# Kernel tuning notes

Measured on AMD Instinct MI355X. Metric: run time of the kernel, lower is better.

## Reference

```python
import jax, jax.numpy as jnp
import numpy as np

B, T, F, H = 256, 1024, 64, 128
DT = 1.0
EPS = 1e-5


def _layer_norm(h, g, b):
    mu = jnp.mean(h, axis=-1, keepdims=True)
    var = jnp.var(h, axis=-1, keepdims=True)
    return (h - mu) * jax.lax.rsqrt(var + EPS) * g + b


def setup_inputs() -> dict:
    key = jax.random.key(0)
    ks = jax.random.split(key, 8)
    def xavier(k, shape):
        fan_in, fan_out = shape[1], shape[0]
        lim = np.sqrt(6.0 / (fan_in + fan_out))
        return jax.random.uniform(k, shape, jnp.float32, -lim, lim)
    return {
        "x": jax.random.normal(ks[0], (B, T, F), jnp.float32),
        # layer 0 (input_dim=F)
        "Wh0": xavier(ks[1], (H, H)), "bh0": jnp.zeros((H,), jnp.float32),
        "Wx0": xavier(ks[2], (H, F)), "bx0": jnp.zeros((H,), jnp.float32),
        "Wt0": xavier(ks[3], (H, F)), "bt0": jnp.zeros((H,), jnp.float32),
        "tau0": jnp.ones((H,), jnp.float32),
        "g0": jnp.ones((H,), jnp.float32), "be0": jnp.zeros((H,), jnp.float32),
        # layer 1 (input_dim=H)
        "Wh1": xavier(ks[4], (H, H)), "bh1": jnp.zeros((H,), jnp.float32),
        "Wx1": xavier(ks[5], (H, H)), "bx1": jnp.zeros((H,), jnp.float32),
        "Wt1": xavier(ks[6], (H, H)), "bt1": jnp.zeros((H,), jnp.float32),
        "tau1": jnp.ones((H,), jnp.float32),
        "g1": jnp.ones((H,), jnp.float32), "be1": jnp.zeros((H,), jnp.float32),
    }


def _cell(x_t, h, Wh, bh, Wx, bx, Wt, bt, tau_base):
    f = jnp.tanh(h @ Wh.T + bh + x_t @ Wx.T + bx)        # (B,H)
    tau = tau_base + jax.nn.softplus(x_t @ Wt.T + bt)     # (B,H)
    return h + (DT / tau) * (-h + f)


def reference(x, Wh0, bh0, Wx0, bx0, Wt0, bt0, tau0, g0, be0,
              Wh1, bh1, Wx1, bx1, Wt1, bt1, tau1, g1, be1):
    xT = jnp.transpose(x, (1, 0, 2))  # (T,B,F)

    def step(carry, x_t):
        h0, h1 = carry
        h0 = _layer_norm(_cell(x_t, h0, Wh0, bh0, Wx0, bx0, Wt0, bt0, tau0), g0, be0)
        h1 = _layer_norm(_cell(h0, h1, Wh1, bh1, Wx1, bx1, Wt1, bt1, tau1), g1, be1)
        return (h0, h1), None

    h_init = (jnp.zeros((x.shape[0], H), x.dtype), jnp.zeros((x.shape[0], H), x.dtype))
    (h0, h1), _ = jax.lax.scan(step, h_init, xT)
    return h1  # hidden_dim == latent_dim, no proj
```

## Files before the change

kernel.cpp:

```cpp
#include <hip/hip_runtime.h>
#include <stdint.h>


#define B_ 256
#define T_ 1024
#define F_ 64
#define H_ 128
#define EPS_ 1e-5f
#define NT_ 512

typedef _Float16 h2 __attribute__((ext_vector_type(2)));
typedef _Float16 h8 __attribute__((ext_vector_type(8)));
typedef float f32x4 __attribute__((ext_vector_type(4)));
typedef __fp16  f16v2 __attribute__((ext_vector_type(2)));

__device__ __forceinline__ h2 pkf16(float a, float b) {
  union { f16v2 f; h2 h; } c;
  c.f = __builtin_amdgcn_cvt_pkrtz(a, b);
  return c.h;
}
__device__ __forceinline__ uint32_t as_u32(h2 h) { union { h2 h; uint32_t u; } c; c.h = h; return c.u; }

__device__ __forceinline__ void wg_barrier() {
  asm volatile("s_waitcnt lgkmcnt(0)\n\ts_barrier" ::: "memory");
}

#if __has_builtin(__builtin_amdgcn_rsqf)
__device__ __forceinline__ float rsq_fast(float x) { return __builtin_amdgcn_rsqf(x); }
#else
__device__ __forceinline__ float rsq_fast(float x) { return rsqrtf(x); }
#endif

#if __has_builtin(__builtin_amdgcn_update_dpp)
template <int CTRL>
__device__ __forceinline__ float dpp_add(float v) {
  union { float f; int i; } a, b;
  a.f = v;
  b.i = __builtin_amdgcn_update_dpp(0, a.i, CTRL, 0xf, 0xf, true);
  return v + b.f;
}
__device__ __forceinline__ float red16(float v) {
  v = dpp_add<0x128>(v);
  v = dpp_add<0x124>(v);
  v = dpp_add<0x122>(v);
  v = dpp_add<0x121>(v);
  return v;
}
#else
__device__ __forceinline__ float red16(float v) {
  v += __shfl_xor(v, 1); v += __shfl_xor(v, 2);
  v += __shfl_xor(v, 4); v += __shfl_xor(v, 8);
  return v;
}
#endif

__device__ __forceinline__ h8 packfrag(const float* p) {
  float4 a = *(const float4*)p;
  float4 b = *(const float4*)(p + 4);
  union { h2 h[4]; h8 v; } c;
  c.h[0] = pkf16(a.x, a.y); c.h[1] = pkf16(a.z, a.w);
  c.h[2] = pkf16(b.x, b.y); c.h[3] = pkf16(b.z, b.w);
  return c.v;
}
__device__ __forceinline__ h8 packfrag_g(const float* w, const float* gv, const float* bv,
                                         float& dg, float& dbe) {
  float4 a = *(const float4*)w;
  float4 b = *(const float4*)(w + 4);
  float4 ga = *(const float4*)gv;
  float4 gb = *(const float4*)(gv + 4);
  float4 ba = *(const float4*)bv;
  float4 bb = *(const float4*)(bv + 4);
  float w0 = a.x*ga.x, w1 = a.y*ga.y, w2 = a.z*ga.z, w3 = a.w*ga.w;
  float w4 = b.x*gb.x, w5 = b.y*gb.y, w6 = b.z*gb.z, w7 = b.w*gb.w;
  dg  += (w0 + w1) + (w2 + w3) + (w4 + w5) + (w6 + w7);
  dbe += a.x*ba.x + a.y*ba.y + a.z*ba.z + a.w*ba.w
       + b.x*bb.x + b.y*bb.y + b.z*bb.z + b.w*bb.w;
  union { h2 h[4]; h8 v; } c;
  c.h[0] = pkf16(w0, w1); c.h[1] = pkf16(w2, w3);
  c.h[2] = pkf16(w4, w5); c.h[3] = pkf16(w6, w7);
  return c.v;
}
__device__ __forceinline__ h8 ldfrag(const uint32_t* p) {
  union { uint4 u; h8 v; } c;
  c.u = *(const uint4*)p;
  return c.v;
}

__device__ __forceinline__ float tanh_fast(float a) {
  float aa = fabsf(a);
  float e  = __expf(2.f * aa);
  float th = 1.f - 2.f * __builtin_amdgcn_rcpf(e + 1.f);
  return copysignf(th, a);
}
__device__ __forceinline__ float softplus_fast(float x) {
  return (x > 20.f) ? x : __logf(1.f + __expf(x));
}

#define MFMA16(A_, B_, C_) __builtin_amdgcn_mfma_f32_16x16x32_f16(A_, B_, C_, 0, 0, 0)

__global__ void __attribute__((amdgpu_flat_work_group_size(NT_, NT_)))
                __attribute__((amdgpu_waves_per_eu(2, 2)))
ltc_scan(
    const float* __restrict__ x,
    const float* __restrict__ Wh0, const float* __restrict__ bh0,
    const float* __restrict__ Wx0, const float* __restrict__ bx0,
    const float* __restrict__ Wt0, const float* __restrict__ bt0,
    const float* __restrict__ tau0, const float* __restrict__ g0,
    const float* __restrict__ be0,
    const float* __restrict__ Wh1, const float* __restrict__ bh1,
    const float* __restrict__ Wx1, const float* __restrict__ bx1,
    const float* __restrict__ Wt1, const float* __restrict__ bt1,
    const float* __restrict__ tau1, const float* __restrict__ g1,
    const float* __restrict__ be1,
    float* __restrict__ out)
{
  __shared__ __align__(16) uint32_t h0p[2][64];
  __shared__ __align__(16) uint32_t h1p[2][64];
  __shared__ __align__(16) uint32_t hn0p[4][64];
  __shared__ __align__(16) uint32_t x4[4][32];
  __shared__ __align__(16) float2   p0s[4][4];
  __shared__ __align__(16) float2   p1s[4][4];

  const int tid = threadIdx.x;
  const int wid = tid >> 6;
  const int l   = tid & 63;
  const int g4  = (l >> 4) << 2;
  const int g8  = (l >> 4) << 3;
  const int b   = blockIdx.x;
  const float* xg = x + (size_t)b * (T_ * F_);
  const bool selT1 = (l & 16) != 0;

  if (tid < 128) { ((uint32_t*)h0p)[tid] = 0u; ((uint32_t*)h1p)[tid] = 0u; }
  if (tid < 32)  { ((float*)p0s)[tid] = 0.f; ((float*)p1s)[tid] = 0.f; }
  if (tid < 32) {
    float2 a = *(const float2*)(xg + 2 * tid);
    float2 c = *(const float2*)(xg + F_ + 2 * tid);
    x4[0][tid] = as_u32(pkf16(a.x, a.y));
    x4[1][tid] = as_u32(pkf16(c.x, c.y));
  }
  __syncthreads();

  if (wid < 4) {
    const int c0 = wid * 32 + (l & 15);
    const int ct = wid * 32 + (l & 31);
    h8 wh0[4], wh1[4], wx0[2], wx1[2], wt0[2], wt1[2];
    float cg, cb;
    {
      float dg0 = 0.f, db0 = 0.f, dg1 = 0.f, db1 = 0.f;
      const float* p0 = Wh0 + c0 * H_ + g8;
      const float* p1 = Wh0 + (c0 + 16) * H_ + g8;
      #pragma unroll
      for (int m = 0; m < 4; ++m) {
        wh0[m] = packfrag_g(p0 + 32 * m, g0 + g8 + 32 * m, be0 + g8 + 32 * m, dg0, db0);
        wh1[m] = packfrag_g(p1 + 32 * m, g0 + g8 + 32 * m, be0 + g8 + 32 * m, dg1, db1);
      }
      dg0 += __shfl_xor(dg0, 16); dg0 += __shfl_xor(dg0, 32);
      db0 += __shfl_xor(db0, 16); db0 += __shfl_xor(db0, 32);
      dg1 += __shfl_xor(dg1, 16); dg1 += __shfl_xor(dg1, 32);
      db1 += __shfl_xor(db1, 16); db1 += __shfl_xor(db1, 32);
      cg = selT1 ? dg1 : dg0; cb = selT1 ? db1 : db0;
      const float* q0 = Wx0 + c0 * F_ + g8;
      const float* q1 = Wx0 + (c0 + 16) * F_ + g8;
      const float* r0 = Wt0 + c0 * F_ + g8;
      const float* r1 = Wt0 + (c0 + 16) * F_ + g8;
      #pragma unroll
      for (int m = 0; m < 2; ++m) {
        wx0[m] = packfrag(q0 + 32 * m); wx1[m] = packfrag(q1 + 32 * m);
        wt0[m] = packfrag(r0 + 32 * m); wt1[m] = packfrag(r1 + 32 * m);
      }
    }
    const float bhx = bh0[ct] + bx0[ct];
    const float btr = bt0[ct], taub = tau0[ct], gr = g0[ct], ber = be0[ct];
    const int  widx = wid * 16 + ((l & 31) >> 1);
    const bool wlane = ((l & 33) == 0);
    const bool st = (wid == 0) && (l < 32);

    float hcp = 0.f;
    float2 xc0, xc1;
    if (st) {
      xc0 = *(const float2*)(xg + 2 * F_ + 2 * l);
      xc1 = *(const float2*)(xg + 3 * F_ + 2 * l);
    }
    float xcs, tcs;
    {
      const uint32_t* xb = x4[0];
      f32x4 nX0 = {0.f,0.f,0.f,0.f}, nX1 = {0.f,0.f,0.f,0.f};
      f32x4 nT0 = {0.f,0.f,0.f,0.f}, nT1 = {0.f,0.f,0.f,0.f};
      #pragma unroll
      for (int m = 0; m < 2; ++m) {
        h8 xf = ldfrag(xb + m * 16 + g4);
        nX0 = MFMA16(xf, wx0[m], nX0);
        nX1 = MFMA16(xf, wx1[m], nX1);
        nT0 = MFMA16(xf, wt0[m], nT0);
        nT1 = MFMA16(xf, wt1[m], nT1);
      }
      xcs = (selT1 ? nX1[0] : nX0[0]) + bhx;
      tcs = (selT1 ? nT1[0] : nT0[0]) + btr;
    }

    #pragma unroll 4
    for (int p = 0; p <= T_ + 2; ++p) {
      if (p <= T_) {
        const int i = p;
        const float4* sp = (const float4*)&p0s[(i + 3) & 3][0];
        float4 sa = sp[0], sb = sp[1];
        float ss  = (sa.x + sa.z) + (sb.x + sb.z);
        float s2s = (sa.y + sa.w) + (sb.y + sb.w);
        if (st) {
          x4[(i + 2) & 3][l] = as_u32(pkf16(xc0.x, xc0.y));
          xc0 = xc1;
          int tn = (i + 4 < T_) ? (i + 4) : (T_ - 1);
          xc1 = *(const float2*)(xg + tn * F_ + 2 * l);
        }
        const uint32_t* ub = h0p[(i + 1) & 1];
        f32x4 aH0a = {0.f,0.f,0.f,0.f}, aH0b = {0.f,0.f,0.f,0.f};
        f32x4 aH1a = {0.f,0.f,0.f,0.f}, aH1b = {0.f,0.f,0.f,0.f};
        {
          h8 af0 = ldfrag(ub + g4);
          h8 af1 = ldfrag(ub + 16 + g4);
          h8 af2 = ldfrag(ub + 32 + g4);
          h8 af3 = ldfrag(ub + 48 + g4);
          aH0a = MFMA16(af0, wh0[0], aH0a); aH1a = MFMA16(af0, wh1[0], aH1a);
          aH0b = MFMA16(af1, wh0[1], aH0b); aH1b = MFMA16(af1, wh1[1], aH1b);
          aH0a = MFMA16(af2, wh0[2], aH0a); aH1a = MFMA16(af2, wh1[2], aH1a);
          aH0b = MFMA16(af3, wh0[3], aH0b); aH1b = MFMA16(af3, wh1[3], aH1b);
        }
        float aH = selT1 ? (aH1a[0] + aH1b[0]) : (aH0a[0] + aH0b[0]);
        float mu = ss * (1.f / 128.f);
        float m2 = s2s * (1.f / 128.f);
        float rstd = rsq_fast(m2 - mu * mu + EPS_);
        float fl = (i > 0) ? 1.f : 0.f;
        float sc = fl * rstd;
        float pa = fmaf(sc, aH, fmaf(-sc * mu, cg, fl * cb)) + xcs;
        float pt = tcs;
        float f   = tanh_fast(pa);
        float tau = taub + softplus_fast(pt);
        float hold = fl * fmaf((hcp - mu) * rstd, gr, ber);
        float hc  = fmaf(f - hold, __builtin_amdgcn_rcpf(tau), hold);
        float hn2 = __shfl_xor(hold, 1);
        if (wlane) hn0p[(i + 3) & 3][widx] = as_u32(pkf16(hold, hn2));
        float hc2 = __shfl_xor(hc, 1);
        if (wlane) h0p[i & 1][widx] = as_u32(pkf16(hc, hc2));
        float v = (l & 32) ? hc * hc : hc;
        v = red16(v); v += __shfl_xor(v, 16);
        float v2 = __shfl_down(v, 32);
        if (l == 0) p0s[i & 3][wid] = make_float2(v, v2);
        hcp = hc;
        {
          const uint32_t* xb = x4[(i + 1) & 3];
          f32x4 nX0 = {0.f,0.f,0.f,0.f}, nX1 = {0.f,0.f,0.f,0.f};
          f32x4 nT0 = {0.f,0.f,0.f,0.f}, nT1 = {0.f,0.f,0.f,0.f};
          #pragma unroll
          for (int m = 0; m < 2; ++m) {
            h8 xf = ldfrag(xb + m * 16 + g4);
            nX0 = MFMA16(xf, wx0[m], nX0);
            nX1 = MFMA16(xf, wx1[m], nX1);
            nT0 = MFMA16(xf, wt0[m], nT0);
            nT1 = MFMA16(xf, wt1[m], nT1);
          }
          xcs = (selT1 ? nX1[0] : nX0[0]) + bhx;
          tcs = (selT1 ? nT1[0] : nT0[0]) + btr;
        }
      }
      wg_barrier();
    }
  } else {
    const int c0 = (wid - 4) * 32 + (l & 15);
    const int ct = (wid - 4) * 32 + (l & 31);
    h8 vh0[4], vh1[4], vx0[4], vx1[4], vt0[4], vt1[4];
    float cAg, cAb;
    {
      float d1 = 0.f, d2 = 0.f, e1 = 0.f, e2 = 0.f;
      const float* p0 = Wh1 + c0 * H_ + g8;
      const float* p1 = Wh1 + (c0 + 16) * H_ + g8;
      const float* q0 = Wx1 + c0 * H_ + g8;
      const float* q1 = Wx1 + (c0 + 16) * H_ + g8;
      const float* r0 = Wt1 + c0 * H_ + g8;
      const float* r1 = Wt1 + (c0 + 16) * H_ + g8;
      #pragma unroll
      for (int m = 0; m < 4; ++m) {
        vh0[m] = packfrag_g(p0 + 32 * m, g1 + g8 + 32 * m, be1 + g8 + 32 * m, d1, d2);
        vh1[m] = packfrag_g(p1 + 32 * m, g1 + g8 + 32 * m, be1 + g8 + 32 * m, e1, e2);
        vx0[m] = packfrag(q0 + 32 * m); vx1[m] = packfrag(q1 + 32 * m);
        vt0[m] = packfrag(r0 + 32 * m); vt1[m] = packfrag(r1 + 32 * m);
      }
      d1 += __shfl_xor(d1, 16); d1 += __shfl_xor(d1, 32);
      d2 += __shfl_xor(d2, 16); d2 += __shfl_xor(d2, 32);
      e1 += __shfl_xor(e1, 16); e1 += __shfl_xor(e1, 32);
      e2 += __shfl_xor(e2, 16); e2 += __shfl_xor(e2, 32);
      cAg = selT1 ? e1 : d1; cAb = selT1 ? e2 : d2;
    }
    const float bhx = bh1[ct] + bx1[ct];
    const float btr = bt1[ct], taub = tau1[ct], gr = g1[ct], ber = be1[ct];
    const int  widx = (wid - 4) * 16 + ((l & 31) >> 1);
    const bool wlane = ((l & 33) == 0);
    const int  bw = wid - 4;

    float hcp = 0.f;
    float bcs = 0.f, tcs = 0.f;
    #pragma unroll 2
    for (int p = 0; p <= T_ + 2; ++p) {
      if (p >= 3) {
        const int j = p - 3;
        const float4* sp = (const float4*)&p1s[(j + 3) & 3][0];
        float4 sa = sp[0], sb = sp[1];
        float ss1 = (sa.x + sa.z) + (sb.x + sb.z);
        float s21 = (sa.y + sa.w) + (sb.y + sb.w);
        const uint32_t* u1b = h1p[(j + 1) & 1];
        f32x4 aA0a = {0.f,0.f,0.f,0.f}, aA0b = {0.f,0.f,0.f,0.f};
        f32x4 aA1a = {0.f,0.f,0.f,0.f}, aA1b = {0.f,0.f,0.f,0.f};
        {
          h8 af0 = ldfrag(u1b + g4);
          h8 af1 = ldfrag(u1b + 16 + g4);
          h8 af2 = ldfrag(u1b + 32 + g4);
          h8 af3 = ldfrag(u1b + 48 + g4);
          aA0a = MFMA16(af0, vh0[0], aA0a); aA1a = MFMA16(af0, vh1[0], aA1a);
          aA0b = MFMA16(af1, vh0[1], aA0b); aA1b = MFMA16(af1, vh1[1], aA1b);
          aA0a = MFMA16(af2, vh0[2], aA0a); aA1a = MFMA16(af2, vh1[2], aA1a);
          aA0b = MFMA16(af3, vh0[3], aA0b); aA1b = MFMA16(af3, vh1[3], aA1b);
        }
        float aA = selT1 ? (aA1a[0] + aA1b[0]) : (aA0a[0] + aA0b[0]);
        float mu1 = ss1 * (1.f / 128.f);
        float m21 = s21 * (1.f / 128.f);
        float rstd1 = rsq_fast(m21 - mu1 * mu1 + EPS_);
        float fl1 = (j > 0) ? 1.f : 0.f;
        float sc1 = fl1 * rstd1;
        float pa = fmaf(sc1, aA, fmaf(-sc1 * mu1, cAg, fl1 * cAb)) + bcs;
        float pt = tcs;
        float f   = tanh_fast(pa);
        float tau = taub + softplus_fast(pt);
        float hold = fl1 * fmaf((hcp - mu1) * rstd1, gr, ber);
        float hc  = fmaf(f - hold, __builtin_amdgcn_rcpf(tau), hold);
        float hc2 = __shfl_xor(hc, 1);
        if (wlane) h1p[j & 1][widx] = as_u32(pkf16(hc, hc2));
        float v = (l & 32) ? hc * hc : hc;
        v = red16(v); v += __shfl_xor(v, 16);
        float v2 = __shfl_down(v, 32);
        if (l == 0) p1s[j & 3][bw] = make_float2(v, v2);
        hcp = hc;
      }
      if (p >= 2 && p <= T_ + 1) {
        const uint32_t* hnb = hn0p[(p - 2) & 3];
        f32x4 nB0 = {0.f,0.f,0.f,0.f}, nB1 = {0.f,0.f,0.f,0.f};
        f32x4 nT0 = {0.f,0.f,0.f,0.f}, nT1 = {0.f,0.f,0.f,0.f};
        #pragma unroll
        for (int m = 0; m < 4; ++m) {
          h8 f0 = ldfrag(hnb + m * 16 + g4);
          nB0 = MFMA16(f0, vx0[m], nB0);
          nB1 = MFMA16(f0, vx1[m], nB1);
          nT0 = MFMA16(f0, vt0[m], nT0);
          nT1 = MFMA16(f0, vt1[m], nT1);
        }
        bcs = (selT1 ? nB1[0] : nB0[0]) + bhx;
        tcs = (selT1 ? nT1[0] : nT0[0]) + btr;
      }
      wg_barrier();
    }
    {
      const float4* sp = (const float4*)&p1s[(T_ - 1) & 3][0];
      float4 sa = sp[0], sb = sp[1];
      float ss1 = (sa.x + sa.z) + (sb.x + sb.z);
      float s21 = (sa.y + sa.w) + (sb.y + sb.w);
      float mu1 = ss1 * (1.f / 128.f);
      float m21 = s21 * (1.f / 128.f);
      float rstd1 = rsq_fast(m21 - mu1 * mu1 + EPS_);
      float hn = fmaf((hcp - mu1) * rstd1, gr, ber);
      if (l < 32) out[b * H_ + ct] = hn;
    }
  }
}

extern "C" void kernel_launch(void* const* d_in, const int* in_sizes, int n_in,
                              void* d_out, int out_size, void* d_ws, size_t ws_size,
                              hipStream_t stream) {
  const float* x    = (const float*)d_in[0];
  const float* Wh0  = (const float*)d_in[1];
  const float* bh0  = (const float*)d_in[2];
  const float* Wx0  = (const float*)d_in[3];
  const float* bx0  = (const float*)d_in[4];
  const float* Wt0  = (const float*)d_in[5];
  const float* bt0  = (const float*)d_in[6];
  const float* tau0 = (const float*)d_in[7];
  const float* g0   = (const float*)d_in[8];
  const float* be0  = (const float*)d_in[9];
  const float* Wh1  = (const float*)d_in[10];
  const float* bh1  = (const float*)d_in[11];
  const float* Wx1  = (const float*)d_in[12];
  const float* bx1  = (const float*)d_in[13];
  const float* Wt1  = (const float*)d_in[14];
  const float* bt1  = (const float*)d_in[15];
  const float* tau1 = (const float*)d_in[16];
  const float* g1   = (const float*)d_in[17];
  const float* be1  = (const float*)d_in[18];
  float* out        = (float*)d_out;

  ltc_scan<<<B_, NT_, 0, stream>>>(x, Wh0, bh0, Wx0, bx0, Wt0, bt0, tau0, g0, be0,
                                   Wh1, bh1, Wx1, bx1, Wt1, bt1, tau1, g1, be1, out);
}
```

Before: 846.3 us.

## Split layer-1 work across eight waves with 16 columns each

Raises the workgroup to 768 threads. Layer 1 now runs on eight waves, each owning 16 output columns, where it used to run on four waves owning 32 columns each. Every layer-1 wave issues half as many MFMAs per step and the select between two column halves goes away, which shortens the per-step critical path of the serial recurrence. The layer-0 LayerNorm partial sums are also reorganised: each 16-lane group writes its own partial and the reader sums more entries, saving two shuffles. The costs are more waves taking part in every barrier, a larger partial-sum reduction at each read, and a waves_per_eu change that may limit registers.

Measured after the change: 928.2 us. 1.1x slower.

```diff
diff --git a/kernel.cpp b/kernel.cpp
--- a/kernel.cpp
+++ b/kernel.cpp
@@ -7,7 +7,7 @@
 #define F_ 64
 #define H_ 128
 #define EPS_ 1e-5f
-#define NT_ 512
+#define NT_ 768
 
 typedef _Float16 h2 __attribute__((ext_vector_type(2)));
 typedef _Float16 h8 __attribute__((ext_vector_type(8)));
@@ -99,7 +99,7 @@
 #define MFMA16(A_, B_, C_) __builtin_amdgcn_mfma_f32_16x16x32_f16(A_, B_, C_, 0, 0, 0)
 
 __global__ void __attribute__((amdgpu_flat_work_group_size(NT_, NT_)))
-                __attribute__((amdgpu_waves_per_eu(2, 2)))
+                __attribute__((amdgpu_waves_per_eu(3, 3)))
 ltc_scan(
     const float* __restrict__ x,
     const float* __restrict__ Wh0, const float* __restrict__ bh0,
@@ -118,8 +118,8 @@
   __shared__ __align__(16) uint32_t h1p[2][64];
   __shared__ __align__(16) uint32_t hn0p[4][64];
   __shared__ __align__(16) uint32_t x4[4][32];
-  __shared__ __align__(16) float2   p0s[4][4];
-  __shared__ __align__(16) float2   p1s[4][4];
+  __shared__ __align__(16) float4   p0s[4][4];
+  __shared__ __align__(16) float2   p1s[4][8];
 
   const int tid = threadIdx.x;
   const int wid = tid >> 6;
@@ -131,7 +131,8 @@
   const bool selT1 = (l & 16) != 0;
 
   if (tid < 128) { ((uint32_t*)h0p)[tid] = 0u; ((uint32_t*)h1p)[tid] = 0u; }
-  if (tid < 32)  { ((float*)p0s)[tid] = 0.f; ((float*)p1s)[tid] = 0.f; }
+  if (tid < 64)  ((float*)p0s)[tid] = 0.f;
+  if (tid >= 64 && tid < 128) ((float*)p1s)[tid - 64] = 0.f;
   if (tid < 32) {
     float2 a = *(const float2*)(xg + 2 * tid);
     float2 c = *(const float2*)(xg + F_ + 2 * tid);
@@ -203,9 +204,9 @@
       if (p <= T_) {
         const int i = p;
         const float4* sp = (const float4*)&p0s[(i + 3) & 3][0];
-        float4 sa = sp[0], sb = sp[1];
-        float ss  = (sa.x + sa.z) + (sb.x + sb.z);
-        float s2s = (sa.y + sa.w) + (sb.y + sb.w);
+        float4 q0 = sp[0], q1 = sp[1], q2 = sp[2], q3 = sp[3];
+        float ss  = (q0.x + q0.y) + (q1.x + q1.y) + (q2.x + q2.y) + (q3.x + q3.y);
+        float s2s = (q0.z + q0.w) + (q1.z + q1.w) + (q2.z + q2.w) + (q3.z + q3.w);
         if (st) {
           x4[(i + 2) & 3][l] = as_u32(pkf16(xc0.x, xc0.y));
           xc0 = xc1;
@@ -242,9 +243,8 @@
         float hc2 = __shfl_xor(hc, 1);
         if (wlane) h0p[i & 1][widx] = as_u32(pkf16(hc, hc2));
         float v = (l & 32) ? hc * hc : hc;
-        v = red16(v); v += __shfl_xor(v, 16);
-        float v2 = __shfl_down(v, 32);
-        if (l == 0) p0s[i & 3][wid] = make_float2(v, v2);
+        v = red16(v);
+        if ((l & 15) == 0) ((float*)&p0s[i & 3][wid])[l >> 4] = v;
         hcp = hc;
         {
           const uint32_t* xb = x4[(i + 1) & 3];
@@ -265,36 +265,29 @@
       wg_barrier();
     }
   } else {
-    const int c0 = (wid - 4) * 32 + (l & 15);
-    const int ct = (wid - 4) * 32 + (l & 31);
-    h8 vh0[4], vh1[4], vx0[4], vx1[4], vt0[4], vt1[4];
+    const int bw = wid - 4;
+    const int ct = bw * 16 + (l & 15);
+    h8 vh[4], vx[4], vt[4];
     float cAg, cAb;
     {
-      float d1 = 0.f, d2 = 0.f, e1 = 0.f, e2 = 0.f;
-      const float* p0 = Wh1 + c0 * H_ + g8;
-      const float* p1 = Wh1 + (c0 + 16) * H_ + g8;
-      const float* q0 = Wx1 + c0 * H_ + g8;
-      const float* q1 = Wx1 + (c0 + 16) * H_ + g8;
-      const float* r0 = Wt1 + c0 * H_ + g8;
-      const float* r1 = Wt1 + (c0 + 16) * H_ + g8;
+      float d1 = 0.f, d2 = 0.f;
+      const float* p0 = Wh1 + ct * H_ + g8;
+      const float* q0 = Wx1 + ct * H_ + g8;
+      const float* r0 = Wt1 + ct * H_ + g8;
       #pragma unroll
       for (int m = 0; m < 4; ++m) {
-        vh0[m] = packfrag_g(p0 + 32 * m, g1 + g8 + 32 * m, be1 + g8 + 32 * m, d1, d2);
-        vh1[m] = packfrag_g(p1 + 32 * m, g1 + g8 + 32 * m, be1 + g8 + 32 * m, e1, e2);
-        vx0[m] = packfrag(q0 + 32 * m); vx1[m] = packfrag(q1 + 32 * m);
-        vt0[m] = packfrag(r0 + 32 * m); vt1[m] = packfrag(r1 + 32 * m);
+        vh[m] = packfrag_g(p0 + 32 * m, g1 + g8 + 32 * m, be1 + g8 + 32 * m, d1, d2);
+        vx[m] = packfrag(q0 + 32 * m);
+        vt[m] = packfrag(r0 + 32 * m);
       }
       d1 += __shfl_xor(d1, 16); d1 += __shfl_xor(d1, 32);
       d2 += __shfl_xor(d2, 16); d2 += __shfl_xor(d2, 32);
-      e1 += __shfl_xor(e1, 16); e1 += __shfl_xor(e1, 32);
-      e2 += __shfl_xor(e2, 16); e2 += __shfl_xor(e2, 32);
-      cAg = selT1 ? e1 : d1; cAb = selT1 ? e2 : d2;
+      cAg = d1; cAb = d2;
     }
     const float bhx = bh1[ct] + bx1[ct];
     const float btr = bt1[ct], taub = tau1[ct], gr = g1[ct], ber = be1[ct];
-    const int  widx = (wid - 4) * 16 + ((l & 31) >> 1);
-    const bool wlane = ((l & 33) == 0);
-    const int  bw = wid - 4;
+    const int  widx = bw * 8 + ((l & 15) >> 1);
+    const bool wlane = ((l & 49) == 0);
 
     float hcp = 0.f;
     float bcs = 0.f, tcs = 0.f;
@@ -303,23 +296,22 @@
       if (p >= 3) {
         const int j = p - 3;
         const float4* sp = (const float4*)&p1s[(j + 3) & 3][0];
-        float4 sa = sp[0], sb = sp[1];
-        float ss1 = (sa.x + sa.z) + (sb.x + sb.z);
-        float s21 = (sa.y + sa.w) + (sb.y + sb.w);
+        float4 s0 = sp[0], s1 = sp[1], s2 = sp[2], s3 = sp[3];
+        float ss1 = (s0.x + s0.z) + (s1.x + s1.z) + (s2.x + s2.z) + (s3.x + s3.z);
+        float s21 = (s0.y + s0.w) + (s1.y + s1.w) + (s2.y + s2.w) + (s3.y + s3.w);
         const uint32_t* u1b = h1p[(j + 1) & 1];
-        f32x4 aA0a = {0.f,0.f,0.f,0.f}, aA0b = {0.f,0.f,0.f,0.f};
-        f32x4 aA1a = {0.f,0.f,0.f,0.f}, aA1b = {0.f,0.f,0.f,0.f};
+        f32x4 aAa = {0.f,0.f,0.f,0.f}, aAb = {0.f,0.f,0.f,0.f};
         {
           h8 af0 = ldfrag(u1b + g4);
           h8 af1 = ldfrag(u1b + 16 + g4);
           h8 af2 = ldfrag(u1b + 32 + g4);
           h8 af3 = ldfrag(u1b + 48 + g4);
-          aA0a = MFMA16(af0, vh0[0], aA0a); aA1a = MFMA16(af0, vh1[0], aA1a);
-          aA0b = MFMA16(af1, vh0[1], aA0b); aA1b = MFMA16(af1, vh1[1], aA1b);
-          aA0a = MFMA16(af2, vh0[2], aA0a); aA1a = MFMA16(af2, vh1[2], aA1a);
-          aA0b = MFMA16(af3, vh0[3], aA0b); aA1b = MFMA16(af3, vh1[3], aA1b);
-        }
-        float aA = selT1 ? (aA1a[0] + aA1b[0]) : (aA0a[0] + aA0b[0]);
+          aAa = MFMA16(af0, vh[0], aAa);
+          aAb = MFMA16(af1, vh[1], aAb);
+          aAa = MFMA16(af2, vh[2], aAa);
+          aAb = MFMA16(af3, vh[3], aAb);
+        }
+        float aA = aAa[0] + aAb[0];
         float mu1 = ss1 * (1.f / 128.f);
         float m21 = s21 * (1.f / 128.f);
         float rstd1 = rsq_fast(m21 - mu1 * mu1 + EPS_);
@@ -334,38 +326,34 @@
         float hc2 = __shfl_xor(hc, 1);
         if (wlane) h1p[j & 1][widx] = as_u32(pkf16(hc, hc2));
         float v = (l & 32) ? hc * hc : hc;
-        v = red16(v); v += __shfl_xor(v, 16);
-        float v2 = __shfl_down(v, 32);
-        if (l == 0) p1s[j & 3][bw] = make_float2(v, v2);
+        v = red16(v);
+        if (l == 0 || l == 32) ((float*)&p1s[j & 3][bw])[l >> 5] = v;
         hcp = hc;
       }
       if (p >= 2 && p <= T_ + 1) {
         const uint32_t* hnb = hn0p[(p - 2) & 3];
-        f32x4 nB0 = {0.f,0.f,0.f,0.f}, nB1 = {0.f,0.f,0.f,0.f};
-        f32x4 nT0 = {0.f,0.f,0.f,0.f}, nT1 = {0.f,0.f,0.f,0.f};
+        f32x4 nB = {0.f,0.f,0.f,0.f}, nT = {0.f,0.f,0.f,0.f};
         #pragma unroll
         for (int m = 0; m < 4; ++m) {
           h8 f0 = ldfrag(hnb + m * 16 + g4);
-          nB0 = MFMA16(f0, vx0[m], nB0);
-          nB1 = MFMA16(f0, vx1[m], nB1);
-          nT0 = MFMA16(f0, vt0[m], nT0);
-          nT1 = MFMA16(f0, vt1[m], nT1);
-        }
-        bcs = (selT1 ? nB1[0] : nB0[0]) + bhx;
-        tcs = (selT1 ? nT1[0] : nT0[0]) + btr;
+          nB = MFMA16(f0, vx[m], nB);
+          nT = MFMA16(f0, vt[m], nT);
+        }
+        bcs = nB[0] + bhx;
+        tcs = nT[0] + btr;
       }
       wg_barrier();
     }
     {
       const float4* sp = (const float4*)&p1s[(T_ - 1) & 3][0];
-      float4 sa = sp[0], sb = sp[1];
-      float ss1 = (sa.x + sa.z) + (sb.x + sb.z);
-      float s21 = (sa.y + sa.w) + (sb.y + sb.w);
+      float4 s0 = sp[0], s1 = sp[1], s2 = sp[2], s3 = sp[3];
+      float ss1 = (s0.x + s0.z) + (s1.x + s1.z) + (s2.x + s2.z) + (s3.x + s3.z);
+      float s21 = (s0.y + s0.w) + (s1.y + s1.w) + (s2.y + s2.w) + (s3.y + s3.w);
       float mu1 = ss1 * (1.f / 128.f);
       float m21 = s21 * (1.f / 128.f);
       float rstd1 = rsq_fast(m21 - mu1 * mu1 + EPS_);
       float hn = fmaf((hcp - mu1) * rstd1, gr, ber);
-      if (l < 32) out[b * H_ + ct] = hn;
+      if (l < 16) out[b * H_ + ct] = hn;
     }
   }
 }
```
